# Kernel tuning notes

Measured on AMD Instinct MI355X. Metric: run time of the kernel, lower is better.

The kernel has to match this reference:

```python
import jax, jax.numpy as jnp
from jax import lax
import numpy as np

PH = PW = 7          # cfg.POOLING_SIZE
SR = 2               # sampling ratio of ROIAlignLayer
SCALE = 1.0 / 16.0   # 1/cfg.FEAT_STRIDE
NCLS = 81
CBASE = 512          # dout_base_model
RCNN_DIN = 4096


def conv(x, w, b, stride):
    y = lax.conv_general_dilated(x, w, (stride, stride), 'SAME',
                                 dimension_numbers=('NCHW', 'OIHW', 'NCHW'))
    return y + b[None, :, None, None]


def roi_align(feat, rois):
    # feat: [C,H,W]; rois: [R,5] (batch_idx, x1,y1,x2,y2) -> [R,C,PH,PW]
    C, H, W = feat.shape
    b = rois[:, 1:5] * SCALE
    x1, y1, x2, y2 = b[:, 0], b[:, 1], b[:, 2], b[:, 3]
    bw = jnp.maximum(x2 - x1, 1.0) / PW
    bh = jnp.maximum(y2 - y1, 1.0) / PH
    gy = y1[:, None] + (jnp.arange(PH * SR, dtype=feat.dtype) + 0.5) / SR * bh[:, None]
    gx = x1[:, None] + (jnp.arange(PW * SR, dtype=feat.dtype) + 0.5) / SR * bw[:, None]
    gy = jnp.clip(gy, 0.0, H - 1)
    gx = jnp.clip(gx, 0.0, W - 1)
    y0f = jnp.floor(gy); x0f = jnp.floor(gx)
    wy = gy - y0f; wx = gx - x0f
    y0 = y0f.astype(jnp.int32); x0 = x0f.astype(jnp.int32)
    y1i = jnp.minimum(y0 + 1, H - 1); x1i = jnp.minimum(x0 + 1, W - 1)
    R, SY = gy.shape; SX = gx.shape[1]
    def gather(yi, xi):
        Y = jnp.broadcast_to(yi[:, :, None], (R, SY, SX))
        X = jnp.broadcast_to(xi[:, None, :], (R, SY, SX))
        return feat[:, Y, X]                      # [C,R,SY,SX]
    wy = wy[None, :, :, None]; wx = wx[None, :, None, :]
    v = (gather(y0, x0) * (1 - wy) * (1 - wx)
         + gather(y0, x1i) * (1 - wy) * wx
         + gather(y1i, x0) * wy * (1 - wx)
         + gather(y1i, x1i) * wy * wx)             # [C,R,SY,SX]
    v = v.reshape(C, R, PH, SR, PW, SR).mean(axis=(3, 5))
    return v.transpose(1, 0, 2, 3)


def setup_inputs() -> dict:
    key = jax.random.key(0)
    ks = jax.random.split(key, 24)
    R = 300
    im_data = jax.random.normal(ks[0], (1, 3, 640, 640), jnp.float32)
    # proposals: batch_idx 0, boxes inside 640x640 image
    x1 = jax.random.uniform(ks[1], (R,)) * 600.0
    y1 = jax.random.uniform(ks[2], (R,)) * 600.0
    x2 = x1 + 16.0 + jax.random.uniform(ks[3], (R,)) * (623.0 - x1)
    y2 = y1 + 16.0 + jax.random.uniform(ks[4], (R,)) * (623.0 - y1)
    rois = jnp.stack([jnp.zeros((R,)), x1, y1, x2, y2], axis=1).astype(jnp.float32)
    s = 0.05
    p = {
        'w1': jax.random.normal(ks[5], (64, 3, 3, 3)) * s,   'b1': jnp.zeros((64,)),
        'w2': jax.random.normal(ks[6], (128, 64, 3, 3)) * s, 'b2': jnp.zeros((128,)),
        'w3': jax.random.normal(ks[7], (256, 128, 3, 3)) * s,'b3': jnp.zeros((256,)),
        'w4': jax.random.normal(ks[8], (CBASE, 256, 3, 3)) * s, 'b4': jnp.zeros((CBASE,)),
        'fc6_w': jax.random.normal(ks[9], (RCNN_DIN, CBASE * PH * PW)) * 0.01,
        'fc6_b': jnp.zeros((RCNN_DIN,)),
        'fc7_w': jax.random.normal(ks[10], (RCNN_DIN, RCNN_DIN)) * 0.01,
        'fc7_b': jnp.zeros((RCNN_DIN,)),
        'cls_w': jax.random.normal(ks[11], (NCLS, RCNN_DIN)) * 0.01,
        'cls_b': jnp.zeros((NCLS,)),
        'bbox_w': jax.random.normal(ks[12], (4 * NCLS, RCNN_DIN)) * 0.001,
        'bbox_b': jnp.zeros((4 * NCLS,)),
    }
    p = {k: v.astype(jnp.float32) for k, v in p.items()}
    return {'im_data': im_data, 'rois': rois, **p}


def reference(im_data, rois, w1, b1, w2, b2, w3, b3, w4, b4,
              fc6_w, fc6_b, fc7_w, fc7_b, cls_w, cls_b, bbox_w, bbox_b):
    # stride-16 backbone (RCNN_base)
    x = jax.nn.relu(conv(im_data, w1, b1, 2))
    x = jax.nn.relu(conv(x, w2, b2, 2))
    x = jax.nn.relu(conv(x, w3, b3, 2))
    base_feat = jax.nn.relu(conv(x, w4, b4, 2))      # [1,512,40,40]
    # ROI align over proposals (batch_size == 1)
    pooled = roi_align(base_feat[0], rois)           # [R,512,7,7]
    R = pooled.shape[0]
    h = pooled.reshape(R, -1)
    h = jax.nn.relu(h @ fc6_w.T + fc6_b)             # fc6_new
    h = jax.nn.relu(h @ fc7_w.T + fc7_b)             # fc7_new
    cls_score = h @ cls_w.T + cls_b
    bbox_pred = h @ bbox_w.T + bbox_b
    cls_prob = jax.nn.softmax(cls_score, axis=1)
    rois_out = rois.reshape(1, R, 5)
    return rois_out, cls_prob.reshape(1, R, -1), bbox_pred.reshape(1, R, -1)
```

## Files before the change

kernel.cpp:

```cpp
#include <hip/hip_runtime.h>
#include <hip/hip_bf16.h>
#include <math.h>

#define R_ROIS 300
#define NCLS 81
#define RCNN_DIN 4096
#define K_FC6 25088
#define FEAT_H 40
#define FEAT_W 40

typedef __attribute__((ext_vector_type(8))) short bf16x8;
typedef __attribute__((ext_vector_type(4))) float f32x4;
typedef __attribute__((ext_vector_type(8))) unsigned short ushort8;
typedef __attribute__((ext_vector_type(4))) unsigned short u16x4;

__device__ inline unsigned short f2bf(float x) {
  union { float f; unsigned u; } v;
  v.f = x;
  unsigned r = v.u + 0x7fff + ((v.u >> 16) & 1);
  return (unsigned short)(r >> 16);
}

template <int CIN, int COPT>
__global__ __launch_bounds__(256) void conv_s2_relu(
    const float* __restrict__ in, const float* __restrict__ w,
    const float* __restrict__ bias, float* __restrict__ out,
    int Hin, int Win, int Hout, int Wout) {
  int pix = blockIdx.x * blockDim.x + threadIdx.x;
  int npix = Hout * Wout;
  if (pix >= npix) return;
  int co0 = blockIdx.y * COPT;
  int oy = pix / Wout, ox = pix % Wout;

  float acc[COPT];
#pragma unroll
  for (int j = 0; j < COPT; ++j) acc[j] = bias[co0 + j];

  for (int cin = 0; cin < CIN; ++cin) {
    const float* ip = in + cin * Hin * Win;
    const float* wp = w + (co0 * CIN + cin) * 9;
#pragma unroll
    for (int ky = 0; ky < 3; ++ky) {
      int iy = oy * 2 + ky;
      if (iy >= Hin) continue;
#pragma unroll
      for (int kx = 0; kx < 3; ++kx) {
        int ix = ox * 2 + kx;
        if (ix >= Win) continue;
        float v = ip[iy * Win + ix];
#pragma unroll
        for (int j = 0; j < COPT; ++j)
          acc[j] = fmaf(v, wp[j * CIN * 9 + ky * 3 + kx], acc[j]);
      }
    }
  }
#pragma unroll
  for (int j = 0; j < COPT; ++j)
    out[(co0 + j) * npix + pix] = fmaxf(acc[j], 0.0f);
}

#define I2C_LSTR 580
__global__ __launch_bounds__(256) void im2col_bf16_staged(
    const float* __restrict__ in, unsigned short* __restrict__ col,
    int Cin, int Hin, int Win, int Hout, int Wout) {
  __shared__ unsigned short lds[32 * I2C_LSTR];
  const int t = threadIdx.x;
  const int pix0 = blockIdx.x * 32;
  const int cin0 = blockIdx.y * 64;

  {
    const int pl = t & 31;
    const int cl = t >> 5;
    const int pix = pix0 + pl;
    const int oy = pix / Wout, ox = pix % Wout;
    for (int cc = cl; cc < 64; cc += 8) {
      const float* ip = in + (size_t)(cin0 + cc) * Hin * Win;
      unsigned short* lp = &lds[pl * I2C_LSTR + cc * 9];
#pragma unroll
      for (int ky = 0; ky < 3; ++ky) {
        int iy = oy * 2 + ky;
#pragma unroll
        for (int kx = 0; kx < 3; ++kx) {
          int ix = ox * 2 + kx;
          float v = (iy < Hin && ix < Win) ? ip[iy * Win + ix] : 0.0f;
          lp[ky * 3 + kx] = f2bf(v);
        }
      }
    }
  }
  __syncthreads();

  const size_t rowstride = (size_t)Cin * 9;
#pragma unroll
  for (int it = 0; it < 18; ++it) {
    int ch = it * 256 + t;
    int row = ch / 144;
    int pos = ch - row * 144;
    u16x4 v = *(const u16x4*)&lds[row * I2C_LSTR + pos * 4];
    *(u16x4*)(col + (size_t)(pix0 + row) * rowstride + cin0 * 9 + pos * 4) = v;
  }
}

__global__ __launch_bounds__(256) void roi_align_kernel(
    const float* __restrict__ feat, const float* __restrict__ rois,
    unsigned short* __restrict__ out) {
  int idx = blockIdx.x * blockDim.x + threadIdx.x;
  if (idx >= R_ROIS * 512 * 49) return;
  int pw = idx % 7;
  int t = idx / 7;
  int ph = t % 7;
  t /= 7;
  int c = t % 512;
  int r = t / 512;

  const float SCALE = 1.0f / 16.0f;
  float x1 = rois[r * 5 + 1] * SCALE;
  float y1 = rois[r * 5 + 2] * SCALE;
  float x2 = rois[r * 5 + 3] * SCALE;
  float y2 = rois[r * 5 + 4] * SCALE;
  float bw = fmaxf(x2 - x1, 1.0f) * (1.0f / 7.0f);
  float bh = fmaxf(y2 - y1, 1.0f) * (1.0f / 7.0f);

  const float* f = feat + c * FEAT_H * FEAT_W;
  float s = 0.0f;
#pragma unroll
  for (int sy = 0; sy < 2; ++sy) {
    float gy = y1 + ((float)(ph * 2 + sy) + 0.5f) * 0.5f * bh;
    gy = fminf(fmaxf(gy, 0.0f), (float)(FEAT_H - 1));
    int y0 = (int)floorf(gy);
    float wy = gy - (float)y0;
    int y1i = min(y0 + 1, FEAT_H - 1);
#pragma unroll
    for (int sx = 0; sx < 2; ++sx) {
      float gx = x1 + ((float)(pw * 2 + sx) + 0.5f) * 0.5f * bw;
      gx = fminf(fmaxf(gx, 0.0f), (float)(FEAT_W - 1));
      int x0 = (int)floorf(gx);
      float wx = gx - (float)x0;
      int x1i = min(x0 + 1, FEAT_W - 1);
      float v00 = f[y0 * FEAT_W + x0];
      float v01 = f[y0 * FEAT_W + x1i];
      float v10 = f[y1i * FEAT_W + x0];
      float v11 = f[y1i * FEAT_W + x1i];
      s += v00 * (1.0f - wy) * (1.0f - wx) + v01 * (1.0f - wy) * wx +
           v10 * wy * (1.0f - wx) + v11 * wy * wx;
    }
  }
  out[idx] = f2bf(s * 0.25f);
}

union RawT {
  float4 f[8];
  ushort8 h[8];
};

__device__ inline void load_f32c(const float* p, size_t K, int row0, int Lim,
                                 RawT& r) {
#pragma unroll
  for (int q = 0; q < 8; ++q) {
    const float4* src = (const float4*)(p + (size_t)(q * 16) * K);
    r.f[q] = (row0 + q * 16 < Lim) ? *src : make_float4(0.f, 0.f, 0.f, 0.f);
  }
}
__device__ inline void load_b16c(const unsigned short* p, size_t K, int row0,
                                 int Lim, RawT& r) {
#pragma unroll
  for (int q = 0; q < 4; ++q) {
    const ushort8* src = (const ushort8*)(p + (size_t)(q * 32) * K);
    r.h[q] = (row0 + q * 32 < Lim) ? *src : (ushort8)0;
  }
}
__device__ inline u16x4 cvt4(float4 a) {
  __hip_bfloat162 p0 = __float22bfloat162_rn(make_float2(a.x, a.y));
  __hip_bfloat162 p1 = __float22bfloat162_rn(make_float2(a.z, a.w));
  u16x4 o;
  o[0] = __bfloat16_as_ushort(p0.x);
  o[1] = __bfloat16_as_ushort(p0.y);
  o[2] = __bfloat16_as_ushort(p1.x);
  o[3] = __bfloat16_as_ushort(p1.y);
  return o;
}

#define LSTR 72
template <bool ABF16, bool BBF16>
__global__ __launch_bounds__(256) void gemm_mfma(
    const void* __restrict__ Ap, const void* __restrict__ Bp,
    float* __restrict__ Cpart, int M, int N, int Kfull, int Ksplit) {
  __shared__ unsigned short As[128 * LSTR];
  __shared__ unsigned short Bs[128 * LSTR];
  const int tid = threadIdx.x;
  const int m0 = blockIdx.y * 128;
  const int n0 = blockIdx.x * 128;
  const int s = blockIdx.z;
  const int k0 = s * Ksplit;

  const int fr32 = tid >> 4;
  const int fc32 = (tid & 15) * 4;
  const int fr16 = tid >> 3;
  const int fc16 = (tid & 7) * 8;

  const int ar0 = m0 + (ABF16 ? fr16 : fr32);
  const int br0 = n0 + (BBF16 ? fr16 : fr32);

  const float* Af = (const float*)Ap + (size_t)ar0 * Kfull + k0 + fc32;
  const unsigned short* Ab =
      (const unsigned short*)Ap + (size_t)ar0 * Kfull + k0 + fc16;
  const float* Bf = (const float*)Bp + (size_t)br0 * Kfull + k0 + fc32;
  const unsigned short* Bb =
      (const unsigned short*)Bp + (size_t)br0 * Kfull + k0 + fc16;

  const int wave = tid >> 6;
  const int lane = tid & 63;
  const int wm = (wave >> 1) * 64;
  const int wn = (wave & 1) * 64;
  const int fm = lane & 15;
  const int fk = (lane >> 4) * 8;

  f32x4 acc[4][4];
#pragma unroll
  for (int i = 0; i < 4; ++i)
#pragma unroll
    for (int j = 0; j < 4; ++j) acc[i][j] = (f32x4)(0.0f);

  RawT ra, rb;
  if (ABF16) load_b16c(Ab, Kfull, ar0, M, ra); else load_f32c(Af, Kfull, ar0, M, ra);
  if (BBF16) load_b16c(Bb, Kfull, br0, N, rb); else load_f32c(Bf, Kfull, br0, N, rb);
  RawT na = ra, nb = rb;

  for (int kt = 0; kt < Ksplit; kt += 64) {
    int ktn = kt + 64;
    if (ktn < Ksplit) {
      if (ABF16) load_b16c(Ab + ktn, Kfull, ar0, M, na);
      else       load_f32c(Af + ktn, Kfull, ar0, M, na);
      if (BBF16) load_b16c(Bb + ktn, Kfull, br0, N, nb);
      else       load_f32c(Bf + ktn, Kfull, br0, N, nb);
    }

    __syncthreads();
    if (ABF16) {
#pragma unroll
      for (int q = 0; q < 4; ++q)
        *(ushort8*)&As[(fr16 + q * 32) * LSTR + fc16] = ra.h[q];
    } else {
#pragma unroll
      for (int q = 0; q < 8; ++q)
        *(u16x4*)&As[(fr32 + q * 16) * LSTR + fc32] = cvt4(ra.f[q]);
    }
    if (BBF16) {
#pragma unroll
      for (int q = 0; q < 4; ++q)
        *(ushort8*)&Bs[(fr16 + q * 32) * LSTR + fc16] = rb.h[q];
    } else {
#pragma unroll
      for (int q = 0; q < 8; ++q)
        *(u16x4*)&Bs[(fr32 + q * 16) * LSTR + fc32] = cvt4(rb.f[q]);
    }
    __syncthreads();

#pragma unroll
    for (int kk = 0; kk < 64; kk += 32) {
      bf16x8 af[4], bfr[4];
#pragma unroll
      for (int i = 0; i < 4; ++i)
        af[i] = *(const bf16x8*)&As[(wm + i * 16 + fm) * LSTR + kk + fk];
#pragma unroll
      for (int j = 0; j < 4; ++j)
        bfr[j] = *(const bf16x8*)&Bs[(wn + j * 16 + fm) * LSTR + kk + fk];
#pragma unroll
      for (int i = 0; i < 4; ++i)
#pragma unroll
        for (int j = 0; j < 4; ++j)
          acc[i][j] = __builtin_amdgcn_mfma_f32_16x16x32_bf16(af[i], bfr[j],
                                                              acc[i][j], 0, 0, 0);
    }
    ra = na;
    rb = nb;
  }

  const int col = lane & 15;
  const int rb4 = (lane >> 4) * 4;
  float* Cp = Cpart + (size_t)s * M * N;
#pragma unroll
  for (int i = 0; i < 4; ++i) {
#pragma unroll
    for (int r = 0; r < 4; ++r) {
      int gm = m0 + wm + i * 16 + rb4 + r;
      if (gm >= M) continue;
#pragma unroll
      for (int j = 0; j < 4; ++j) {
        int gn = n0 + wn + j * 16 + col;
        if (gn < N) Cp[(size_t)gm * N + gn] = acc[i][j][r];
      }
    }
  }
}

__global__ __launch_bounds__(256) void finalize_kernel(
    const float* __restrict__ part, const float* __restrict__ bias,
    void* __restrict__ out, int M, int N, int S, int bias_on_n, int relu,
    int out_bf16) {
  int idx = blockIdx.x * blockDim.x + threadIdx.x;
  if (idx >= M * N) return;
  int m = idx / N;
  int n = idx - m * N;
  float v = 0.0f;
  for (int s2 = 0; s2 < S; ++s2) v += part[(size_t)s2 * M * N + idx];
  v += bias[bias_on_n ? n : m];
  if (relu) v = fmaxf(v, 0.0f);
  if (out_bf16)
    ((unsigned short*)out)[idx] = f2bf(v);
  else
    ((float*)out)[idx] = v;
}

__global__ __launch_bounds__(128) void softmax81(const float* __restrict__ in,
                                                 float* __restrict__ out) {
  int r = blockIdx.x * blockDim.x + threadIdx.x;
  if (r >= R_ROIS) return;
  const float* x = in + r * NCLS;
  float m = -1e30f;
  for (int i = 0; i < NCLS; ++i) m = fmaxf(m, x[i]);
  float s = 0.0f;
  for (int i = 0; i < NCLS; ++i) s += expf(x[i] - m);
  float inv = 1.0f / s;
  float* o = out + r * NCLS;
  for (int i = 0; i < NCLS; ++i) o[i] = expf(x[i] - m) * inv;
}

__global__ __launch_bounds__(256) void copy_rois(const float* __restrict__ rois,
                                                 float* __restrict__ out) {
  int i = blockIdx.x * blockDim.x + threadIdx.x;
  if (i < R_ROIS * 5) out[i] = rois[i];
}

extern "C" void kernel_launch(void* const* d_in, const int* in_sizes, int n_in,
                              void* d_out, int out_size, void* d_ws,
                              size_t ws_size, hipStream_t stream) {
  const float* im = (const float*)d_in[0];
  const float* rois = (const float*)d_in[1];
  const float* w1 = (const float*)d_in[2];
  const float* b1 = (const float*)d_in[3];
  const float* w2 = (const float*)d_in[4];
  const float* b2 = (const float*)d_in[5];
  const float* w3 = (const float*)d_in[6];
  const float* b3 = (const float*)d_in[7];
  const float* w4 = (const float*)d_in[8];
  const float* b4 = (const float*)d_in[9];
  const float* fc6_w = (const float*)d_in[10];
  const float* fc6_b = (const float*)d_in[11];
  const float* fc7_w = (const float*)d_in[12];
  const float* fc7_b = (const float*)d_in[13];
  const float* cls_w = (const float*)d_in[14];
  const float* cls_b = (const float*)d_in[15];
  const float* bbox_w = (const float*)d_in[16];
  const float* bbox_b = (const float*)d_in[17];

  float* ws = (float*)d_ws;
  float* x1 = ws;
  float* x2 = ws + 6553600;
  float* x3 = ws + 9830400;
  float* x4 = ws + 11468800;
  unsigned short* col = (unsigned short*)(ws + 12288000);
  float* cpart = ws + 19660800;
  float* cpart_fc = ws + 5120000;
  unsigned short* pooledb = (unsigned short*)ws;
  unsigned short* h6b = (unsigned short*)(ws + 3763200);
  unsigned short* h7b = (unsigned short*)(ws + 4377600);
  float* cls_score = ws + 4992000;

  float* out = (float*)d_out;
  float* out_rois = out;
  float* out_cls = out + 1500;
  float* out_bbox = out + 25800;

  conv_s2_relu<3, 4><<<dim3(400, 16), 256, 0, stream>>>(im, w1, b1, x1, 640,
                                                        640, 320, 320);

  im2col_bf16_staged<<<dim3(800, 1), 256, 0, stream>>>(x1, col, 64, 320, 320,
                                                       160, 160);
  gemm_mfma<false, true><<<dim3(200, 1, 1), 256, 0, stream>>>(
      w2, col, cpart, 128, 25600, 576, 576);
  finalize_kernel<<<dim3(12800), 256, 0, stream>>>(cpart, b2, x2, 128, 25600,
                                                   1, 0, 1, 0);

  im2col_bf16_staged<<<dim3(200, 2), 256, 0, stream>>>(x2, col, 128, 160, 160,
                                                       80, 80);
  gemm_mfma<false, true><<<dim3(50, 2, 2), 256, 0, stream>>>(
      w3, col, cpart, 256, 6400, 1152, 576);
  finalize_kernel<<<dim3(6400), 256, 0, stream>>>(cpart, b3, x3, 256, 6400, 2,
                                                  0, 1, 0);

  im2col_bf16_staged<<<dim3(50, 4), 256, 0, stream>>>(x3, col, 256, 80, 80,
                                                      40, 40);
  gemm_mfma<false, true><<<dim3(13, 4, 4), 256, 0, stream>>>(
      w4, col, cpart, 512, 1600, 2304, 576);
  finalize_kernel<<<dim3(3200), 256, 0, stream>>>(cpart, b4, x4, 512, 1600, 4,
                                                  0, 1, 0);

  roi_align_kernel<<<dim3(29400), 256, 0, stream>>>(x4, rois, pooledb);

  gemm_mfma<true, false><<<dim3(32, 3, 14), 256, 0, stream>>>(
      pooledb, fc6_w, cpart_fc, 300, 4096, 25088, 1792);
  finalize_kernel<<<dim3(4800), 256, 0, stream>>>(cpart_fc, fc6_b, h6b, 300,
                                                  4096, 14, 1, 1, 1);

  gemm_mfma<true, false><<<dim3(32, 3, 8), 256, 0, stream>>>(
      h6b, fc7_w, cpart_fc, 300, 4096, 4096, 512);
  finalize_kernel<<<dim3(4800), 256, 0, stream>>>(cpart_fc, fc7_b, h7b, 300,
                                                  4096, 8, 1, 1, 1);

  gemm_mfma<true, false><<<dim3(1, 3, 16), 256, 0, stream>>>(
      h7b, cls_w, cpart, 300, 81, 4096, 256);
  finalize_kernel<<<dim3(95), 256, 0, stream>>>(cpart, cls_b, cls_score, 300,
                                                81, 16, 1, 0, 0);

  gemm_mfma<true, false><<<dim3(3, 3, 16), 256, 0, stream>>>(
      h7b, bbox_w, cpart, 300, 324, 4096, 256);
  finalize_kernel<<<dim3(380), 256, 0, stream>>>(cpart, bbox_b, out_bbox, 300,
                                                 324, 16, 1, 0, 0);

  softmax81<<<dim3(3), 128, 0, stream>>>(cls_score, out_cls);
  copy_rois<<<dim3(6), 256, 0, stream>>>(rois, out_rois);
}
```

Measured before the change: 1.018 ms.

## Fuse bias+ReLU into conv GEMMs, merge head GEMMs, cut launches and splits

The conv GEMMs drop split-K and apply bias and ReLU in the epilogue, which removes three finalize kernels and their partial-buffer round trips. The cls and bbox heads are merged into one GEMM over a concatenated output dimension with a single finalize, and the ROI copy is folded into the softmax kernel. The fc6 split-K factor is reduced and the first conv processes more output channels per block. Fewer splits mean less parallelism for the conv3/conv4 GEMMs, which now launch only tens of blocks.

```diff
diff --git a/kernel.cpp b/kernel.cpp
--- a/kernel.cpp
+++ b/kernel.cpp
@@ -8,6 +8,7 @@
 #define K_FC6 25088
 #define FEAT_H 40
 #define FEAT_W 40
+#define N_HEADS 405
 
 typedef __attribute__((ext_vector_type(8))) short bf16x8;
 typedef __attribute__((ext_vector_type(4))) float f32x4;
@@ -184,7 +185,8 @@
 template <bool ABF16, bool BBF16>
 __global__ __launch_bounds__(256) void gemm_mfma(
     const void* __restrict__ Ap, const void* __restrict__ Bp,
-    float* __restrict__ Cpart, int M, int N, int Kfull, int Ksplit) {
+    float* __restrict__ Cpart, int M, int N, int Kfull, int Ksplit,
+    const float* __restrict__ bias_m) {
   __shared__ unsigned short As[128 * LSTR];
   __shared__ unsigned short Bs[128 * LSTR];
   const int tid = threadIdx.x;
@@ -285,13 +287,125 @@
     for (int r = 0; r < 4; ++r) {
       int gm = m0 + wm + i * 16 + rb4 + r;
       if (gm >= M) continue;
+      float bv = bias_m ? bias_m[gm] : 0.0f;
 #pragma unroll
       for (int j = 0; j < 4; ++j) {
         int gn = n0 + wn + j * 16 + col;
-        if (gn < N) Cp[(size_t)gm * N + gn] = acc[i][j][r];
+        if (gn < N) {
+          float v = acc[i][j][r];
+          if (bias_m) v = fmaxf(v + bv, 0.0f);
+          Cp[(size_t)gm * N + gn] = v;
+        }
       }
     }
   }
+}
+
+__global__ __launch_bounds__(256) void gemm_heads(
+    const unsigned short* __restrict__ Ab_, const float* __restrict__ cls_w,
+    const float* __restrict__ bbox_w, float* __restrict__ Cpart, int Ksplit) {
+  __shared__ unsigned short As[128 * LSTR];
+  __shared__ unsigned short Bs[128 * LSTR];
+  const int tid = threadIdx.x;
+  const int m0 = blockIdx.y * 128;
+  const int n0 = blockIdx.x * 128;
+  const int s = blockIdx.z;
+  const int k0 = s * Ksplit;
+  const int K = RCNN_DIN;
+
+  const int fr32 = tid >> 4;
+  const int fc32 = (tid & 15) * 4;
+  const int fr16 = tid >> 3;
+  const int fc16 = (tid & 7) * 8;
+
+  const int ar0 = m0 + fr16;
+  const unsigned short* Ab = Ab_ + (size_t)ar0 * K + k0 + fc16;
+
+  const int wave = tid >> 6;
+  const int lane = tid & 63;
+  const int wm = (wave >> 1) * 64;
+  const int wn = (wave & 1) * 64;
+  const int fm = lane & 15;
+  const int fk = (lane >> 4) * 8;
+
+  f32x4 acc[4][4];
+#pragma unroll
+  for (int i = 0; i < 4; ++i)
+#pragma unroll
+    for (int j = 0; j < 4; ++j) acc[i][j] = (f32x4)(0.0f);
+
+  for (int kt = 0; kt < Ksplit; kt += 64) {
+    RawT ra, rb;
+    load_b16c(Ab + kt, K, ar0, R_ROIS, ra);
+#pragma unroll
+    for (int q = 0; q < 8; ++q) {
+      int row = n0 + fr32 + q * 16;
+      const float* bp = (row < NCLS) ? cls_w + (size_t)row * K
+                                     : bbox_w + (size_t)(row - NCLS) * K;
+      rb.f[q] = (row < N_HEADS) ? *(const float4*)(bp + k0 + kt + fc32)
+                                : make_float4(0.f, 0.f, 0.f, 0.f);
+    }
+
+    __syncthreads();
+#pragma unroll
+    for (int q = 0; q < 4; ++q)
+      *(ushort8*)&As[(fr16 + q * 32) * LSTR + fc16] = ra.h[q];
+#pragma unroll
+    for (int q = 0; q < 8; ++q)
+      *(u16x4*)&Bs[(fr32 + q * 16) * LSTR + fc32] = cvt4(rb.f[q]);
+    __syncthreads();
+
+#pragma unroll
+    for (int kk = 0; kk < 64; kk += 32) {
+      bf16x8 af[4], bfr[4];
+#pragma unroll
+      for (int i = 0; i < 4; ++i)
+        af[i] = *(const bf16x8*)&As[(wm + i * 16 + fm) * LSTR + kk + fk];
+#pragma unroll
+      for (int j = 0; j < 4; ++j)
+        bfr[j] = *(const bf16x8*)&Bs[(wn + j * 16 + fm) * LSTR + kk + fk];
+#pragma unroll
+      for (int i = 0; i < 4; ++i)
+#pragma unroll
+        for (int j = 0; j < 4; ++j)
+          acc[i][j] = __builtin_amdgcn_mfma_f32_16x16x32_bf16(af[i], bfr[j],
+                                                              acc[i][j], 0, 0, 0);
+    }
+    __syncthreads();
+  }
+
+  const int col = lane & 15;
+  const int rb4 = (lane >> 4) * 4;
+  float* Cp = Cpart + (size_t)s * R_ROIS * N_HEADS;
+#pragma unroll
+  for (int i = 0; i < 4; ++i) {
+#pragma unroll
+    for (int r = 0; r < 4; ++r) {
+      int gm = m0 + wm + i * 16 + rb4 + r;
+      if (gm >= R_ROIS) continue;
+#pragma unroll
+      for (int j = 0; j < 4; ++j) {
+        int gn = n0 + wn + j * 16 + col;
+        if (gn < N_HEADS) Cp[(size_t)gm * N_HEADS + gn] = acc[i][j][r];
+      }
+    }
+  }
+}
+
+__global__ __launch_bounds__(256) void finalize_heads(
+    const float* __restrict__ part, const float* __restrict__ cls_b,
+    const float* __restrict__ bbox_b, float* __restrict__ cls_score,
+    float* __restrict__ out_bbox, int S) {
+  int idx = blockIdx.x * blockDim.x + threadIdx.x;
+  if (idx >= R_ROIS * N_HEADS) return;
+  int m = idx / N_HEADS;
+  int n = idx - m * N_HEADS;
+  float v = 0.0f;
+  for (int s2 = 0; s2 < S; ++s2) v += part[(size_t)s2 * R_ROIS * N_HEADS + idx];
+  if (n < NCLS)
+    cls_score[m * NCLS + n] = v + cls_b[n];
+  else
+    out_bbox[m * (N_HEADS - NCLS) + (n - NCLS)] = v + bbox_b[n - NCLS];
 }
 
 __global__ __launch_bounds__(256) void finalize_kernel(
@@ -312,9 +426,11 @@
     ((float*)out)[idx] = v;
 }
 
-__global__ __launch_bounds__(128) void softmax81(const float* __restrict__ in,
-                                                 float* __restrict__ out) {
+__global__ __launch_bounds__(128) void softmax81_rois(
+    const float* __restrict__ in, float* __restrict__ out,
+    const float* __restrict__ rois, float* __restrict__ out_rois) {
   int r = blockIdx.x * blockDim.x + threadIdx.x;
+  for (int i = r; i < R_ROIS * 5; i += 384) out_rois[i] = rois[i];
   if (r >= R_ROIS) return;
   const float* x = in + r * NCLS;
   float m = -1e30f;
@@ -324,12 +440,6 @@
   float inv = 1.0f / s;
   float* o = out + r * NCLS;
   for (int i = 0; i < NCLS; ++i) o[i] = expf(x[i] - m) * inv;
-}
-
-__global__ __launch_bounds__(256) void copy_rois(const float* __restrict__ rois,
-                                                 float* __restrict__ out) {
-  int i = blockIdx.x * blockDim.x + threadIdx.x;
-  if (i < R_ROIS * 5) out[i] = rois[i];
 }
 
 extern "C" void kernel_launch(void* const* d_in, const int* in_sizes, int n_in,
@@ -372,52 +482,41 @@
   float* out_cls = out + 1500;
   float* out_bbox = out + 25800;
 
-  conv_s2_relu<3, 4><<<dim3(400, 16), 256, 0, stream>>>(im, w1, b1, x1, 640,
+  conv_s2_relu<3, 16><<<dim3(400, 4), 256, 0, stream>>>(im, w1, b1, x1, 640,
                                                         640, 320, 320);
 
   im2col_bf16_staged<<<dim3(800, 1), 256, 0, stream>>>(x1, col, 64, 320, 320,
                                                        160, 160);
   gemm_mfma<false, true><<<dim3(200, 1, 1), 256, 0, stream>>>(
-      w2, col, cpart, 128, 25600, 576, 576);
-  finalize_kernel<<<dim3(12800), 256, 0, stream>>>(cpart, b2, x2, 128, 25600,
-                                                   1, 0, 1, 0);
+      w2, col, x2, 128, 25600, 576, 576, b2);
 
   im2col_bf16_staged<<<dim3(200, 2), 256, 0, stream>>>(x2, col, 128, 160, 160,
                                                        80, 80);
-  gemm_mfma<false, true><<<dim3(50, 2, 2), 256, 0, stream>>>(
-      w3, col, cpart, 256, 6400, 1152, 576);
-  finalize_kernel<<<dim3(6400), 256, 0, stream>>>(cpart, b3, x3, 256, 6400, 2,
-                                                  0, 1, 0);
+  gemm_mfma<false, true><<<dim3(50, 2, 1), 256, 0, stream>>>(
+      w3, col, x3, 256, 6400, 1152, 1152, b3);
 
   im2col_bf16_staged<<<dim3(50, 4), 256, 0, stream>>>(x3, col, 256, 80, 80,
                                                       40, 40);
-  gemm_mfma<false, true><<<dim3(13, 4, 4), 256, 0, stream>>>(
-      w4, col, cpart, 512, 1600, 2304, 576);
-  finalize_kernel<<<dim3(3200), 256, 0, stream>>>(cpart, b4, x4, 512, 1600, 4,
-                                                  0, 1, 0);
+  gemm_mfma<false, true><<<dim3(13, 4, 1), 256, 0, stream>>>(
+      w4, col, x4, 512, 1600, 2304, 2304, b4);
 
   roi_align_kernel<<<dim3(29400), 256, 0, stream>>>(x4, rois, pooledb);
 
-  gemm_mfma<true, false><<<dim3(32, 3, 14), 256, 0, stream>>>(
-      pooledb, fc6_w, cpart_fc, 300, 4096, 25088, 1792);
+  gemm_mfma<true, false><<<dim3(32, 3, 8), 256, 0, stream>>>(
+      pooledb, fc6_w, cpart_fc, 300, 4096, 25088, 3136, nullptr);
   finalize_kernel<<<dim3(4800), 256, 0, stream>>>(cpart_fc, fc6_b, h6b, 300,
-                                                  4096, 14, 1, 1, 1);
+                                                  4096, 8, 1, 1, 1);
 
   gemm_mfma<true, false><<<dim3(32, 3, 8), 256, 0, stream>>>(
-      h6b, fc7_w, cpart_fc, 300, 4096, 4096, 512);
+      h6b, fc7_w, cpart_fc, 300, 4096, 4096, 512, nullptr);
   finalize_kernel<<<dim3(4800), 256, 0, stream>>>(cpart_fc, fc7_b, h7b, 300,
                                                   4096, 8, 1, 1, 1);
 
-  gemm_mfma<true, false><<<dim3(1, 3, 16), 256, 0, stream>>>(
-      h7b, cls_w, cpart, 300, 81, 4096, 256);
-  finalize_kernel<<<dim3(95), 256, 0, stream>>>(cpart, cls_b, cls_score, 300,
-                                                81, 16, 1, 0, 0);
-
-  gemm_mfma<true, false><<<dim3(3, 3, 16), 256, 0, stream>>>(
-      h7b, bbox_w, cpart, 300, 324, 4096, 256);
-  finalize_kernel<<<dim3(380), 256, 0, stream>>>(cpart, bbox_b, out_bbox, 300,
-                                                 324, 16, 1, 0, 0);
-
-  softmax81<<<dim3(3), 128, 0, stream>>>(cls_score, out_cls);
-  copy_rois<<<dim3(6), 256, 0, stream>>>(rois, out_rois);
-}
+  gemm_heads<<<dim3(4, 3, 8), 256, 0, stream>>>(h7b, cls_w, bbox_w, cpart,
+                                                512);
+  finalize_heads<<<dim3(475), 256, 0, stream>>>(cpart, cls_b, bbox_b,
+                                                cls_score, out_bbox, 8);
+
+  softmax81_rois<<<dim3(3), 128, 0, stream>>>(cls_score, out_cls, rois,
+                                              out_rois);
+}
```

New measurement: 1.098 ms. +7.8%, slower.
